# Kernel tuning notes

Hardware: AMD Instinct MI355X
Metric: run time of the kernel (lower is better)

Reference implementation:

```python
import jax, jax.numpy as jnp
import numpy as np

N, F, H, C, B = 50000, 128, 128, 32, 512
E = 600000


def _norm_edges(edge_index, n):
    # PyG GCNConv default: add self-loops, symmetric normalization
    src = jnp.concatenate([edge_index[0], jnp.arange(n, dtype=edge_index.dtype)])
    dst = jnp.concatenate([edge_index[1], jnp.arange(n, dtype=edge_index.dtype)])
    deg = jax.ops.segment_sum(jnp.ones_like(dst, dtype=jnp.float32), dst, num_segments=n)
    inv_sqrt = jnp.where(deg > 0, jax.lax.rsqrt(jnp.maximum(deg, 1.0)), 0.0)
    norm = inv_sqrt[src] * inv_sqrt[dst]  # [E+N]
    return src, dst, norm


def _gcn_conv(x, W, b, src, dst, norm, n):
    h = x @ W                                  # [N, H] dense transform
    msg = norm[:, None] * h[src]               # gather + per-edge scale
    out = jax.ops.segment_sum(msg, dst, num_segments=n)  # scatter-add
    return out + b


def setup_inputs() -> dict:
    key = jax.random.key(0)
    ks = jax.random.split(key, 20)
    x = jax.random.normal(ks[0], (N, F), dtype=jnp.float32)
    edge_index = jax.random.randint(ks[1], (2, E), 0, N, dtype=jnp.int64)
    batch = jnp.sort(jax.random.randint(ks[2], (N,), 0, B, dtype=jnp.int64))
    d = {"x": x, "edge_index": edge_index, "batch": batch}
    dims_in = [F, H, H, H, H, H]
    for i in range(6):
        s = 1.0 / np.sqrt(dims_in[i])
        d[f"W{i+1}"] = jax.random.uniform(ks[3 + i], (dims_in[i], H), jnp.float32, -s, s)
        d[f"b{i+1}"] = jnp.zeros((H,), jnp.float32)
    s = 1.0 / np.sqrt(H)
    d["lin_W"] = jax.random.uniform(ks[10], (H, C), jnp.float32, -s, s)
    d["lin_b"] = jnp.zeros((C,), jnp.float32)
    return d


def reference(x, edge_index, batch, W1, b1, W2, b2, W3, b3, W4, b4, W5, b5, W6, b6, lin_W, lin_b):
    n = x.shape[0]
    src, dst, norm = _norm_edges(edge_index, n)
    Ws = [W1, W2, W3, W4, W5, W6]
    bs = [b1, b2, b3, b4, b5, b6]
    h = x
    for i in range(6):
        h = _gcn_conv(h, Ws[i], bs[i], src, dst, norm, n)
        if i < 5:
            h = jax.nn.relu(h)
    # global mean pool over graph ids
    counts = jax.ops.segment_sum(jnp.ones((n,), jnp.float32), batch, num_segments=B)
    pooled = jax.ops.segment_sum(h, batch, num_segments=B) / jnp.maximum(counts, 1.0)[:, None]
    # dropout is identity in eval mode
    return pooled @ lin_W + lin_b
```

## Files before the change

kernel.cpp:

```cpp
#include <hip/hip_runtime.h>
#include <hip/hip_fp16.h>


static inline int ceil_div(int a, int b) { return (a + b - 1) / b; }

typedef _Float16 f16x8 __attribute__((ext_vector_type(8)));
typedef _Float16 f16x4 __attribute__((ext_vector_type(4)));
typedef float f32x4 __attribute__((ext_vector_type(4)));


__global__ __launch_bounds__(256) void hist_i32(const int* __restrict__ idx,
                                                int* __restrict__ cnt, int n) {
  int i = blockIdx.x * 256 + threadIdx.x;
  if (i < n) atomicAdd(&cnt[idx[i]], 1);
}

__global__ __launch_bounds__(256) void inv_sqrt_deg(const int* __restrict__ deg,
                                                    float* __restrict__ inv, int n) {
  int i = blockIdx.x * 256 + threadIdx.x;
  if (i < n) inv[i] = rsqrtf((float)(deg[i] + 1));
}

__global__ __launch_bounds__(256) void scanA(const int* __restrict__ deg,
                                             int* __restrict__ tmp,
                                             int* __restrict__ sums, int n) {
  __shared__ int s[256];
  int t = threadIdx.x;
  int gid = blockIdx.x * 256 + t;
  s[t] = (gid < n) ? deg[gid] : 0;
  __syncthreads();
  for (int off = 1; off < 256; off <<= 1) {
    int add = (t >= off) ? s[t - off] : 0;
    __syncthreads();
    s[t] += add;
    __syncthreads();
  }
  if (gid < n) tmp[gid] = s[t];
  if (t == 255) sums[blockIdx.x] = s[255];
}

__global__ __launch_bounds__(256) void scanB(int* __restrict__ sums, int nchunk) {
  __shared__ int s[256];
  int t = threadIdx.x;
  s[t] = (t < nchunk) ? sums[t] : 0;
  __syncthreads();
  for (int off = 1; off < 256; off <<= 1) {
    int add = (t >= off) ? s[t - off] : 0;
    __syncthreads();
    s[t] += add;
    __syncthreads();
  }
  if (t < nchunk) sums[t] = s[t];
}

__global__ __launch_bounds__(256) void scanC(const int* __restrict__ tmp,
                                             const int* __restrict__ sums,
                                             int* __restrict__ rp, int n) {
  int gid = blockIdx.x * 256 + threadIdx.x;
  if (gid < n) {
    int off = (blockIdx.x > 0) ? sums[blockIdx.x - 1] : 0;
    rp[gid + 1] = tmp[gid] + off;
    if (gid == 0) rp[0] = 0;
  }
}

__global__ __launch_bounds__(256) void bsearch_starts(const int* __restrict__ batch,
                                                      int* __restrict__ gstart,
                                                      int n, int B) {
  int g = blockIdx.x * 256 + threadIdx.x;
  if (g > B) return;
  int lo = 0, hi = n;
  while (lo < hi) {
    int mid = (lo + hi) >> 1;
    if (batch[mid] < g) lo = mid + 1; else hi = mid;
  }
  gstart[g] = lo;
}

__global__ __launch_bounds__(256) void scatter_edges(const int* __restrict__ src,
                                                     const int* __restrict__ dst,
                                                     int* __restrict__ cursor,
                                                     int* __restrict__ col, int E) {
  int i = blockIdx.x * 256 + threadIdx.x;
  if (i < E) {
    int d = dst[i];
    int pos = atomicAdd(&cursor[d], 1);
    col[pos] = src[i];
  }
}

__global__ __launch_bounds__(256) void f32_to_f16(const float* __restrict__ in,
                                                  _Float16* __restrict__ out, int n) {
  int i = (blockIdx.x * 256 + threadIdx.x) * 4;
  if (i < n) {
    float4 v = *(const float4*)&in[i];
    f16x4 o = {(_Float16)v.x, (_Float16)v.y, (_Float16)v.z, (_Float16)v.w};
    *(f16x4*)&out[i] = o;
  }
}

struct WP { const float* p[6]; };
__global__ __launch_bounds__(256) void conv_weights(WP wp, _Float16* __restrict__ wt) {
  int wi = blockIdx.x >> 6;
  int e = (blockIdx.x & 63) * 256 + threadIdx.x;
  int k = e >> 7, c = e & 127;
  wt[((size_t)wi << 14) + (size_t)c * 128 + k] = (_Float16)wp.p[wi][e];
}


__global__ __launch_bounds__(256, 2) void gemm_mfma_p(const _Float16* __restrict__ A,
                                                      const _Float16* __restrict__ Wt,
                                                      const float* __restrict__ inv,
                                                      _Float16* __restrict__ out,
                                                      int nrows) {
  int lane = threadIdx.x & 63;
  int wv = threadIdx.x >> 6;
  int r = lane & 15, g = lane >> 4;

  f16x8 b[8][4];
  const _Float16* bp = Wt + (size_t)r * 128 + g * 8;
#pragma unroll
  for (int ct = 0; ct < 8; ++ct) {
    const _Float16* bt = bp + (size_t)ct * 16 * 128;
#pragma unroll
    for (int ks = 0; ks < 4; ++ks) b[ct][ks] = *(const f16x8*)(bt + ks * 32);
  }

  int tiles = (nrows + 15) >> 4;
  int chunk = (tiles + gridDim.x - 1) / (int)gridDim.x;
  int t0 = blockIdx.x * chunk;
  int t1 = t0 + chunk;
  if (t1 > tiles) t1 = tiles;

  for (int tt = t0 + wv; tt < t1; tt += 4) {
    int rowBase = tt * 16;

    int arow = rowBase + r;
    if (arow >= nrows) arow = nrows - 1;
    const _Float16* ap = A + (size_t)arow * 128 + g * 8;
    f16x8 a0 = *(const f16x8*)(ap + 0);
    f16x8 a1 = *(const f16x8*)(ap + 32);
    f16x8 a2 = *(const f16x8*)(ap + 64);
    f16x8 a3 = *(const f16x8*)(ap + 96);

    f32x4 acc[8];
#pragma unroll
    for (int ct = 0; ct < 8; ++ct) acc[ct] = (f32x4){0.f, 0.f, 0.f, 0.f};

#pragma unroll
    for (int ct = 0; ct < 8; ++ct) {
      acc[ct] = __builtin_amdgcn_mfma_f32_16x16x32_f16(a0, b[ct][0], acc[ct], 0, 0, 0);
      acc[ct] = __builtin_amdgcn_mfma_f32_16x16x32_f16(a1, b[ct][1], acc[ct], 0, 0, 0);
      acc[ct] = __builtin_amdgcn_mfma_f32_16x16x32_f16(a2, b[ct][2], acc[ct], 0, 0, 0);
      acc[ct] = __builtin_amdgcn_mfma_f32_16x16x32_f16(a3, b[ct][3], acc[ct], 0, 0, 0);
    }

#pragma unroll
    for (int j = 0; j < 4; ++j) {
      int row = rowBase + g * 4 + j;
      if (row < nrows) {
        float iv = inv[row];
#pragma unroll
        for (int ct = 0; ct < 8; ++ct)
          out[(size_t)row * 128 + ct * 16 + r] = (_Float16)(acc[ct][j] * iv);
      }
    }
  }
}

__global__ __launch_bounds__(256) void aggregate(const __half* __restrict__ hs,
                                                 const int* __restrict__ col,
                                                 const int* __restrict__ rp,
                                                 const float* __restrict__ inv,
                                                 const float* __restrict__ bias,
                                                 __half* __restrict__ out, int n,
                                                 int dorelu) {
  int node = blockIdx.x * 4 + (threadIdx.x >> 6);
  if (node >= n) return;
  int lane = threadIdx.x & 63;
  const __half2* h2 = (const __half2*)hs;

  int beg = rp[node], end = rp[node + 1];
  float2 self = __half22float2(h2[(size_t)node * 64 + lane]);
  float sx[8], sy[8];
  sx[0] = self.x; sy[0] = self.y;
#pragma unroll
  for (int i = 1; i < 8; ++i) { sx[i] = 0.f; sy[i] = 0.f; }

  int e = beg;
  for (; e + 8 <= end; e += 8) {
    int idx[8];
#pragma unroll
    for (int i = 0; i < 8; ++i) idx[i] = col[e + i];
    __half2 v[8];
#pragma unroll
    for (int i = 0; i < 8; ++i) v[i] = h2[(size_t)idx[i] * 64 + lane];
#pragma unroll
    for (int i = 0; i < 8; ++i) {
      float2 f = __half22float2(v[i]);
      sx[i] += f.x; sy[i] += f.y;
    }
  }
  if (e + 4 <= end) {
    int idx[4];
#pragma unroll
    for (int i = 0; i < 4; ++i) idx[i] = col[e + i];
    __half2 v[4];
#pragma unroll
    for (int i = 0; i < 4; ++i) v[i] = h2[(size_t)idx[i] * 64 + lane];
#pragma unroll
    for (int i = 0; i < 4; ++i) {
      float2 f = __half22float2(v[i]);
      sx[i] += f.x; sy[i] += f.y;
    }
    e += 4;
  }
  for (; e < end; ++e) {
    int s = col[e];
    float2 f = __half22float2(h2[(size_t)s * 64 + lane]);
    sx[0] += f.x; sy[0] += f.y;
  }

  float ax = (sx[0] + sx[1]) + (sx[2] + sx[3]);
  float bx = (sx[4] + sx[5]) + (sx[6] + sx[7]);
  float ay = (sy[0] + sy[1]) + (sy[2] + sy[3]);
  float by = (sy[4] + sy[5]) + (sy[6] + sy[7]);

  float iv = inv[node];
  float rx = iv * (ax + bx) + bias[lane * 2 + 0];
  float ry = iv * (ay + by) + bias[lane * 2 + 1];
  if (dorelu) { rx = fmaxf(rx, 0.f); ry = fmaxf(ry, 0.f); }
  ((__half2*)out)[(size_t)node * 64 + lane] = __floats2half2_rn(rx, ry);
}

__global__ __launch_bounds__(128) void pool_mean(const __half* __restrict__ h,
                                                 const int* __restrict__ gstart,
                                                 float* __restrict__ pooled) {
  int g = blockIdx.x;
  int c = threadIdx.x;
  int s = gstart[g], e = gstart[g + 1];
  float acc = 0.f;
  for (int v = s; v < e; ++v) acc += __half2float(h[(size_t)v * 128 + c]);
  int cnt = e - s;
  pooled[(size_t)g * 128 + c] = acc / (float)(cnt > 0 ? cnt : 1);
}

__global__ __launch_bounds__(256) void final_lin(const float* __restrict__ pooled,
                                                 const float* __restrict__ lw,
                                                 const float* __restrict__ lb,
                                                 float* __restrict__ out, int total) {
  int idx = blockIdx.x * 256 + threadIdx.x;
  if (idx >= total) return;
  int g = idx >> 5;
  int c = idx & 31;
  float s = 0.f;
#pragma unroll 8
  for (int k = 0; k < 128; ++k) s += pooled[(size_t)g * 128 + k] * lw[k * 32 + c];
  out[idx] = s + lb[c];
}


extern "C" void kernel_launch(void* const* d_in, const int* in_sizes, int n_in,
                              void* d_out, int out_size, void* d_ws, size_t ws_size,
                              hipStream_t stream) {
  const float* x = (const float*)d_in[0];
  const int* ei = (const int*)d_in[1];
  const int* batch = (const int*)d_in[2];
  WP wp;
  const float* bvec[6];
  for (int i = 0; i < 6; ++i) {
    wp.p[i] = (const float*)d_in[3 + 2 * i];
    bvec[i] = (const float*)d_in[4 + 2 * i];
  }
  const float* linW = (const float*)d_in[15];
  const float* linb = (const float*)d_in[16];
  float* out = (float*)d_out;

  const int F = 128, H = 128, C = 32;
  const int N = in_sizes[0] / F;
  const int E = in_sizes[1] / 2;
  const int B = out_size / C;
  const int* src = ei;
  const int* dst = ei + E;

  char* w = (char*)d_ws;
  auto alloc = [&](size_t bytes) -> char* {
    char* p = w;
    w += (bytes + 255) & ~(size_t)255;
    return p;
  };
  int* deg = (int*)alloc((size_t)N * 4);
  float* inv = (float*)alloc((size_t)N * 4);
  int* tmp = (int*)alloc((size_t)N * 4);
  int* sums = (int*)alloc(256 * 4);
  int* rp = (int*)alloc((size_t)(N + 1) * 4);
  int* cursor = (int*)alloc((size_t)N * 4);
  int* col = (int*)alloc((size_t)E * 4);
  int* gstart = (int*)alloc((size_t)(B + 1) * 4);
  _Float16* h16 = (_Float16*)alloc((size_t)N * H * 2);
  _Float16* hs16 = (_Float16*)alloc((size_t)N * H * 2);
  _Float16* wt16 = (_Float16*)alloc((size_t)6 * H * H * 2);
  float* pooled = (float*)alloc((size_t)B * H * 4);
  (void)n_in; (void)ws_size;

  hipMemsetAsync(deg, 0, (size_t)N * 4, stream);

  hist_i32<<<ceil_div(E, 256), 256, 0, stream>>>(dst, deg, E);
  inv_sqrt_deg<<<ceil_div(N, 256), 256, 0, stream>>>(deg, inv, N);

  int nchunk = ceil_div(N, 256);
  scanA<<<nchunk, 256, 0, stream>>>(deg, tmp, sums, N);
  scanB<<<1, 256, 0, stream>>>(sums, nchunk);
  scanC<<<nchunk, 256, 0, stream>>>(tmp, sums, rp, N);
  bsearch_starts<<<ceil_div(B + 1, 256), 256, 0, stream>>>(batch, gstart, N, B);

  hipMemcpyAsync(cursor, rp, (size_t)N * 4, hipMemcpyDeviceToDevice, stream);
  scatter_edges<<<ceil_div(E, 256), 256, 0, stream>>>(src, dst, cursor, col, E);

  f32_to_f16<<<ceil_div(N * F / 4, 256), 256, 0, stream>>>(x, h16, N * F);
  conv_weights<<<384, 256, 0, stream>>>(wp, wt16);

  for (int l = 0; l < 6; ++l) {
    gemm_mfma_p<<<512, 256, 0, stream>>>(h16, wt16 + ((size_t)l << 14), inv, hs16, N);
    aggregate<<<ceil_div(N, 4), 256, 0, stream>>>((const __half*)hs16, col, rp, inv,
                                                  bvec[l], (__half*)h16, N,
                                                  (l < 5) ? 1 : 0);
  }

  pool_mean<<<B, 128, 0, stream>>>((const __half*)h16, gstart, pooled);
  final_lin<<<ceil_div(B * C, 256), 256, 0, stream>>>(pooled, linW, linb, out, B * C);
}
```

Before: 496.7 us.

## Fuse setup kernels, drop cursor memcpy, and vectorize GEMM output stores

Folds the inverse-sqrt-degree computation into scanA and has scanC write the scatter cursor directly, which removes a kernel launch and a device memcpy. The f32-to-f16 conversion, weight transpose and graph-start binary search are merged into one multi-role launch. The GEMM swaps MFMA operand order so each lane holds four consecutive output columns, allowing 8-byte vector stores instead of scalar half stores. It also switches the GEMM to a grid-stride tile loop. These mostly cut launch overhead and store transactions, at the cost of more complex kernels.

```diff
diff --git a/kernel.cpp b/kernel.cpp
--- a/kernel.cpp
+++ b/kernel.cpp
@@ -15,19 +15,16 @@
   if (i < n) atomicAdd(&cnt[idx[i]], 1);
 }
 
-__global__ __launch_bounds__(256) void inv_sqrt_deg(const int* __restrict__ deg,
-                                                    float* __restrict__ inv, int n) {
-  int i = blockIdx.x * 256 + threadIdx.x;
-  if (i < n) inv[i] = rsqrtf((float)(deg[i] + 1));
-}
-
 __global__ __launch_bounds__(256) void scanA(const int* __restrict__ deg,
                                              int* __restrict__ tmp,
-                                             int* __restrict__ sums, int n) {
+                                             int* __restrict__ sums,
+                                             float* __restrict__ inv, int n) {
   __shared__ int s[256];
   int t = threadIdx.x;
   int gid = blockIdx.x * 256 + t;
-  s[t] = (gid < n) ? deg[gid] : 0;
+  int d = (gid < n) ? deg[gid] : 0;
+  if (gid < n) inv[gid] = rsqrtf((float)(d + 1));
+  s[t] = d;
   __syncthreads();
   for (int off = 1; off < 256; off <<= 1) {
     int add = (t >= off) ? s[t - off] : 0;
@@ -55,26 +52,17 @@
 
 __global__ __launch_bounds__(256) void scanC(const int* __restrict__ tmp,
                                              const int* __restrict__ sums,
-                                             int* __restrict__ rp, int n) {
+                                             const int* __restrict__ deg,
+                                             int* __restrict__ rp,
+                                             int* __restrict__ cursor, int n) {
   int gid = blockIdx.x * 256 + threadIdx.x;
   if (gid < n) {
     int off = (blockIdx.x > 0) ? sums[blockIdx.x - 1] : 0;
-    rp[gid + 1] = tmp[gid] + off;
+    int incl = tmp[gid] + off;
+    rp[gid + 1] = incl;
+    cursor[gid] = incl - deg[gid];
     if (gid == 0) rp[0] = 0;
   }
-}
-
-__global__ __launch_bounds__(256) void bsearch_starts(const int* __restrict__ batch,
-                                                      int* __restrict__ gstart,
-                                                      int n, int B) {
-  int g = blockIdx.x * 256 + threadIdx.x;
-  if (g > B) return;
-  int lo = 0, hi = n;
-  while (lo < hi) {
-    int mid = (lo + hi) >> 1;
-    if (batch[mid] < g) lo = mid + 1; else hi = mid;
-  }
-  gstart[g] = lo;
 }
 
 __global__ __launch_bounds__(256) void scatter_edges(const int* __restrict__ src,
@@ -89,22 +77,39 @@
   }
 }
 
-__global__ __launch_bounds__(256) void f32_to_f16(const float* __restrict__ in,
-                                                  _Float16* __restrict__ out, int n) {
-  int i = (blockIdx.x * 256 + threadIdx.x) * 4;
-  if (i < n) {
-    float4 v = *(const float4*)&in[i];
-    f16x4 o = {(_Float16)v.x, (_Float16)v.y, (_Float16)v.z, (_Float16)v.w};
-    *(f16x4*)&out[i] = o;
-  }
-}
-
 struct WP { const float* p[6]; };
-__global__ __launch_bounds__(256) void conv_weights(WP wp, _Float16* __restrict__ wt) {
-  int wi = blockIdx.x >> 6;
-  int e = (blockIdx.x & 63) * 256 + threadIdx.x;
-  int k = e >> 7, c = e & 127;
-  wt[((size_t)wi << 14) + (size_t)c * 128 + k] = (_Float16)wp.p[wi][e];
+__global__ __launch_bounds__(256) void setup_fuse(const float* __restrict__ x,
+                                                  _Float16* __restrict__ h16,
+                                                  WP wp, _Float16* __restrict__ wt,
+                                                  const int* __restrict__ batch,
+                                                  int* __restrict__ gstart,
+                                                  int nelem, int nodes, int B,
+                                                  int nbF) {
+  int blk = blockIdx.x;
+  if (blk < nbF) {
+    int i = (blk * 256 + threadIdx.x) * 4;
+    if (i < nelem) {
+      float4 v = *(const float4*)&x[i];
+      f16x4 o = {(_Float16)v.x, (_Float16)v.y, (_Float16)v.z, (_Float16)v.w};
+      *(f16x4*)&h16[i] = o;
+    }
+  } else if (blk < nbF + 384) {
+    int b2 = blk - nbF;
+    int wi = b2 >> 6;
+    int e = (b2 & 63) * 256 + threadIdx.x;
+    int k = e >> 7, c = e & 127;
+    wt[((size_t)wi << 14) + (size_t)c * 128 + k] = (_Float16)wp.p[wi][e];
+  } else {
+    int g = (blk - nbF - 384) * 256 + threadIdx.x;
+    if (g <= B) {
+      int lo = 0, hi = nodes;
+      while (lo < hi) {
+        int mid = (lo + hi) >> 1;
+        if (batch[mid] < g) lo = mid + 1; else hi = mid;
+      }
+      gstart[g] = lo;
+    }
+  }
 }
 
 
@@ -127,12 +132,8 @@
   }
 
   int tiles = (nrows + 15) >> 4;
-  int chunk = (tiles + gridDim.x - 1) / (int)gridDim.x;
-  int t0 = blockIdx.x * chunk;
-  int t1 = t0 + chunk;
-  if (t1 > tiles) t1 = tiles;
-
-  for (int tt = t0 + wv; tt < t1; tt += 4) {
+  int nwaves = (int)gridDim.x * 4;
+  for (int tt = blockIdx.x * 4 + wv; tt < tiles; tt += nwaves) {
     int rowBase = tt * 16;
 
     int arow = rowBase + r;
@@ -149,20 +150,24 @@
 
 #pragma unroll
     for (int ct = 0; ct < 8; ++ct) {
-      acc[ct] = __builtin_amdgcn_mfma_f32_16x16x32_f16(a0, b[ct][0], acc[ct], 0, 0, 0);
-      acc[ct] = __builtin_amdgcn_mfma_f32_16x16x32_f16(a1, b[ct][1], acc[ct], 0, 0, 0);
-      acc[ct] = __builtin_amdgcn_mfma_f32_16x16x32_f16(a2, b[ct][2], acc[ct], 0, 0, 0);
-      acc[ct] = __builtin_amdgcn_mfma_f32_16x16x32_f16(a3, b[ct][3], acc[ct], 0, 0, 0);
-    }
-
-#pragma unroll
-    for (int j = 0; j < 4; ++j) {
-      int row = rowBase + g * 4 + j;
-      if (row < nrows) {
-        float iv = inv[row];
-#pragma unroll
-        for (int ct = 0; ct < 8; ++ct)
-          out[(size_t)row * 128 + ct * 16 + r] = (_Float16)(acc[ct][j] * iv);
+      acc[ct] = __builtin_amdgcn_mfma_f32_16x16x32_f16(b[ct][0], a0, acc[ct], 0, 0, 0);
+      acc[ct] = __builtin_amdgcn_mfma_f32_16x16x32_f16(b[ct][1], a1, acc[ct], 0, 0, 0);
+      acc[ct] = __builtin_amdgcn_mfma_f32_16x16x32_f16(b[ct][2], a2, acc[ct], 0, 0, 0);
+      acc[ct] = __builtin_amdgcn_mfma_f32_16x16x32_f16(b[ct][3], a3, acc[ct], 0, 0, 0);
+    }
+
+    int node = rowBase + r;
+    if (node < nrows) {
+      float iv = inv[node];
+      _Float16* op = out + (size_t)node * 128 + g * 4;
+#pragma unroll
+      for (int ct = 0; ct < 8; ++ct) {
+        __half2 lo = __floats2half2_rn(acc[ct][0] * iv, acc[ct][1] * iv);
+        __half2 hi = __floats2half2_rn(acc[ct][2] * iv, acc[ct][3] * iv);
+        uint2 sv;
+        sv.x = *(unsigned*)&lo;
+        sv.y = *(unsigned*)&hi;
+        *(uint2*)(op + ct * 16) = sv;
       }
     }
   }
@@ -306,19 +311,18 @@
   hipMemsetAsync(deg, 0, (size_t)N * 4, stream);
 
   hist_i32<<<ceil_div(E, 256), 256, 0, stream>>>(dst, deg, E);
-  inv_sqrt_deg<<<ceil_div(N, 256), 256, 0, stream>>>(deg, inv, N);
 
   int nchunk = ceil_div(N, 256);
-  scanA<<<nchunk, 256, 0, stream>>>(deg, tmp, sums, N);
+  scanA<<<nchunk, 256, 0, stream>>>(deg, tmp, sums, inv, N);
   scanB<<<1, 256, 0, stream>>>(sums, nchunk);
-  scanC<<<nchunk, 256, 0, stream>>>(tmp, sums, rp, N);
-  bsearch_starts<<<ceil_div(B + 1, 256), 256, 0, stream>>>(batch, gstart, N, B);
-
-  hipMemcpyAsync(cursor, rp, (size_t)N * 4, hipMemcpyDeviceToDevice, stream);
+  scanC<<<nchunk, 256, 0, stream>>>(tmp, sums, deg, rp, cursor, N);
+
+  int nbF = ceil_div(N * F / 4, 256);
+  int nbBS = ceil_div(B + 1, 256);
+  setup_fuse<<<nbF + 384 + nbBS, 256, 0, stream>>>(x, h16, wp, wt16, batch, gstart,
+                                                   N * F, N, B, nbF);
+
   scatter_edges<<<ceil_div(E, 256), 256, 0, stream>>>(src, dst, cursor, col, E);
-
-  f32_to_f16<<<ceil_div(N * F / 4, 256), 256, 0, stream>>>(x, h16, N * F);
-  conv_weights<<<384, 256, 0, stream>>>(wp, wt16);
 
   for (int l = 0; l < 6; ++l) {
     gemm_mfma_p<<<512, 256, 0, stream>>>(h16, wt16 + ((size_t)l << 14), inv, hs16, N);
```

New measurement: 493.3 us. About the same (-0.7%).
